# Performance work log

Hardware: AMD Instinct MI355X
Metric: run time of the kernel (lower is better)

The kernel has to match this reference:

```python
import jax, jax.numpy as jnp
import numpy as np

B, S, D, H, DH = 2, 2048, 1024, 16, 64
GLOBAL_RATIO = 0.1
LN_EPS = 1e-5


def setup_inputs() -> dict:
    key = jax.random.key(0)
    ks = jax.random.split(key, 8)
    w = lambda k, shape: jax.random.normal(k, shape, jnp.float32) * 0.02
    return {
        'x': jax.random.normal(ks[0], (B, S, D), jnp.float32),
        'Wq': w(ks[1], (D, H * DH)),
        'Wk': w(ks[2], (D, H * DH)),
        'Wv': w(ks[3], (D, H * DH)),
        'Wo': w(ks[4], (H * DH, D)),
        'bo': jnp.zeros((D,), jnp.float32),
        'ln_gamma': jnp.ones((DH,), jnp.float32),
        'ln_beta': jnp.zeros((DH,), jnp.float32),
        'Wg': w(ks[5], (2 * DH, DH)),
        'bg': jnp.zeros((DH,), jnp.float32),
    }


def _layernorm(x, gamma, beta):
    mu = jnp.mean(x, axis=-1, keepdims=True)
    var = jnp.mean(jnp.square(x - mu), axis=-1, keepdims=True)
    return (x - mu) * jax.lax.rsqrt(var + LN_EPS) * gamma + beta


def reference(x, Wq, Wk, Wv, Wo, bo, ln_gamma, ln_beta, Wg, bg):
    b, s, _ = x.shape
    # projections -> [b, h, n, d]
    split = lambda t: t.reshape(b, s, H, DH).transpose(0, 2, 1, 3)
    q = split(x @ Wq)
    k = split(x @ Wk)
    v = split(x @ Wv)
    scale = DH ** -0.5

    # local (full) attention: manual QK^T / softmax / AV
    scores = jnp.einsum('bhnd,bhmd->bhnm', q, k) * scale  # [b,h,s,s]
    attn = jax.nn.softmax(scores, axis=-1)
    local_out = jnp.einsum('bhnm,bhmd->bhnd', attn, v)

    # cross-segment fusion: top-k keys by norm per (b, h)
    num_global = max(1, int(s * GLOBAL_RATIO))
    key_norms = jnp.linalg.norm(k, axis=-1)  # [b,h,s]
    _, top_idx = jax.lax.top_k(key_norms, num_global)  # [b,h,g]
    idx = top_idx[..., None]  # [b,h,g,1]
    global_k = jnp.take_along_axis(k, idx, axis=2)  # [b,h,g,d]
    global_v = jnp.take_along_axis(v, idx, axis=2)
    g_scores = jnp.einsum('bhnd,bhgd->bhng', q, global_k) * scale
    g_attn = jax.nn.softmax(g_scores, axis=-1)
    global_out = jnp.einsum('bhng,bhgd->bhnd', g_attn, global_v)
    global_out = _layernorm(global_out, ln_gamma, ln_beta)

    # learned gate over [local, global]
    cat = jnp.concatenate([local_out, global_out], axis=-1)  # [b,h,s,2d]
    gate = jax.nn.sigmoid(cat @ Wg + bg)
    fused = gate * local_out + (1.0 - gate) * global_out

    out = fused.transpose(0, 2, 1, 3).reshape(b, s, H * DH)  # b h n d -> b n (h d)
    return out @ Wo + bo
```

## Files before the change

kernel.cpp:

```cpp
#include <hip/hip_runtime.h>


constexpr int SEQ    = 2048;
constexpr int DMODEL = 1024;
constexpr int NH     = 16;
constexpr int DHEAD  = 64;
constexpr int BHT    = 32;
constexpr int NG     = 204;
constexpr int NGPAD  = 256;
constexpr float LNEPS = 1e-5f;

typedef __attribute__((ext_vector_type(8))) short short8;
typedef __attribute__((ext_vector_type(4))) short short4v;
typedef __attribute__((ext_vector_type(4))) float f32x4;

__device__ __forceinline__ unsigned short f2bf(float f) {
    unsigned int u = __float_as_uint(f);
    u += 0x7FFFu + ((u >> 16) & 1u);
    return (unsigned short)(u >> 16);
}
__device__ __forceinline__ float bf2f(unsigned short b) {
    return __uint_as_float(((unsigned int)b) << 16);
}

__global__ __launch_bounds__(256)
void prep_k(const float* __restrict__ x,
            const float* __restrict__ Wq, const float* __restrict__ Wv,
            const float* __restrict__ Wo, const float* __restrict__ Wk,
            const float* __restrict__ Wg,
            unsigned short* __restrict__ xh, unsigned short* __restrict__ xl,
            unsigned short* __restrict__ Wqt, unsigned short* __restrict__ Wvt,
            unsigned short* __restrict__ Wot, unsigned short* __restrict__ Wkh,
            unsigned short* __restrict__ Wkl, unsigned short* __restrict__ Wgt)
{
    const int bid = blockIdx.x;
    const int tid = threadIdx.x;

    if (bid < 2048) {
        int i = (bid * 256 + tid) << 3;
        short8 h, l;
#pragma unroll
        for (int j = 0; j < 8; ++j) {
            float v = x[i + j];
            unsigned short hb = f2bf(v);
            h[j] = (short)hb;
            l[j] = (short)f2bf(v - bf2f(hb));
        }
        *(short8*)(xh + i) = h;
        *(short8*)(xl + i) = l;
        return;
    }
    if (bid == 3072) {
#pragma unroll
        for (int i = 0; i < 32; ++i) {
            int o = tid * 32 + i;
            int dg = o >> 7, jj = o & 127;
            Wgt[o] = f2bf(Wg[jj * 64 + dg]);
        }
        return;
    }

    __shared__ float tile[64][68];
    const int sub = bid - 2048;
    const int which = sub >> 8;
    const int b = sub & 255;
    const int n0 = (b & 15) * 64, k0 = (b >> 4) * 64;
    const float* W = (which == 0) ? Wq : (which == 1) ? Wv : (which == 2) ? Wo : Wk;
    const int Kd = DMODEL, Nd = DMODEL;

#pragma unroll
    for (int p = 0; p < 4; ++p) {
        int c = tid + (p << 8);
        int r = c >> 4, c4 = (c & 15) << 2;
        *(float4*)&tile[r][c4] = *(const float4*)(W + (size_t)(k0 + r) * Nd + n0 + c4);
    }
    __syncthreads();
#pragma unroll
    for (int p = 0; p < 4; ++p) {
        int c = tid + (p << 8);
        int n = c >> 4, k4 = (c & 15) << 2;
        if (which < 3) {
            unsigned short* Wt = (which == 0) ? Wqt : (which == 1) ? Wvt : Wot;
            short4v o;
#pragma unroll
            for (int j = 0; j < 4; ++j) o[j] = (short)f2bf(tile[k4 + j][n]);
            *(short4v*)(Wt + (size_t)(n0 + n) * Kd + k0 + k4) = o;
        } else {
            short4v oh, ol;
#pragma unroll
            for (int j = 0; j < 4; ++j) {
                float v = tile[k4 + j][n];
                unsigned short hb = f2bf(v);
                oh[j] = (short)hb;
                ol[j] = (short)f2bf(v - bf2f(hb));
            }
            *(short4v*)(Wkh + (size_t)(n0 + n) * Kd + k0 + k4) = oh;
            *(short4v*)(Wkl + (size_t)(n0 + n) * Kd + k0 + k4) = ol;
        }
    }
}

__global__ __launch_bounds__(512)
void gemm_bf16_k(const unsigned short* __restrict__ A,
                 const unsigned short* __restrict__ Bt,
                 const float* __restrict__ bias,
                 void* __restrict__ outv, void* __restrict__ outv2,
                 unsigned short* __restrict__ vtout,
                 int M, int N, int K, int mode)
{
    __shared__ __align__(16) unsigned short As[128][72];
    __shared__ __align__(16) unsigned short Bs[128][72];
    const int tid = threadIdx.x;
    const int lane = tid & 63, wave = tid >> 6;
    const int quad = lane >> 4, ln = lane & 15;
    const int mh = (wave >> 2) << 6;
    const int nh = (wave & 3) << 5;
    const int m0 = blockIdx.y * 128, n0 = blockIdx.x * 128;

    f32x4 acc[4][2];
#pragma unroll
    for (int i = 0; i < 4; ++i)
#pragma unroll
        for (int j = 0; j < 2; ++j) acc[i][j] = (f32x4){0.f, 0.f, 0.f, 0.f};

    short8 areg[2], breg[2];
#pragma unroll
    for (int p = 0; p < 2; ++p) {
        int c = tid + (p << 9);
        int row = c >> 3, col8 = (c & 7) << 3;
        areg[p] = *(const short8*)(A + (size_t)(m0 + row) * K + col8);
        breg[p] = *(const short8*)(Bt + (size_t)(n0 + row) * K + col8);
    }

    for (int k0 = 0; k0 < K; k0 += 64) {
        __syncthreads();
#pragma unroll
        for (int p = 0; p < 2; ++p) {
            int c = tid + (p << 9);
            int row = c >> 3, col8 = (c & 7) << 3;
            *(short8*)&As[row][col8] = areg[p];
            *(short8*)&Bs[row][col8] = breg[p];
        }
        __syncthreads();
        if (k0 + 64 < K) {
#pragma unroll
            for (int p = 0; p < 2; ++p) {
                int c = tid + (p << 9);
                int row = c >> 3, col8 = (c & 7) << 3;
                areg[p] = *(const short8*)(A + (size_t)(m0 + row) * K + k0 + 64 + col8);
                breg[p] = *(const short8*)(Bt + (size_t)(n0 + row) * K + k0 + 64 + col8);
            }
        }
#pragma unroll
        for (int ch = 0; ch < 2; ++ch) {
            short8 af[4], bf[2];
#pragma unroll
            for (int mt = 0; mt < 4; ++mt)
                af[mt] = *(const short8*)&As[mh + mt * 16 + ln][ch * 32 + quad * 8];
#pragma unroll
            for (int nt = 0; nt < 2; ++nt)
                bf[nt] = *(const short8*)&Bs[nh + nt * 16 + ln][ch * 32 + quad * 8];
#pragma unroll
            for (int mt = 0; mt < 4; ++mt)
#pragma unroll
                for (int nt = 0; nt < 2; ++nt)
                    acc[mt][nt] = __builtin_amdgcn_mfma_f32_16x16x32_bf16(
                        af[mt], bf[nt], acc[mt][nt], 0, 0, 0);
        }
    }

    if (mode == 0) {
        float* out = (float*)outv;
#pragma unroll
        for (int mt = 0; mt < 4; ++mt)
#pragma unroll
            for (int nt = 0; nt < 2; ++nt)
#pragma unroll
                for (int r = 0; r < 4; ++r) {
                    int m = m0 + mh + mt * 16 + quad * 4 + r;
                    int n = n0 + nh + nt * 16 + ln;
                    out[(size_t)m * N + n] = acc[mt][nt][r] + bias[n];
                }
    } else {
#pragma unroll
        for (int mt = 0; mt < 4; ++mt)
#pragma unroll
            for (int nt = 0; nt < 2; ++nt) {
                int n = n0 + nh + nt * 16 + ln;
                int mb = m0 + mh + mt * 16 + quad * 4;
                int b = mb >> 11, s0 = mb & (SEQ - 1);
                int d = n & 63;
                if (n < DMODEL) {
                    int h = n >> 6;
                    unsigned short* qp_ =
                        (unsigned short*)outv + ((size_t)(b * NH + h) * SEQ + s0) * DHEAD + d;
#pragma unroll
                    for (int r = 0; r < 4; ++r)
                        qp_[(size_t)r * DHEAD] = f2bf(acc[mt][nt][r] * 0.18033688f);
                } else {
                    int h = (n >> 6) - NH;
                    unsigned short* vp_ =
                        (unsigned short*)outv2 + ((size_t)(b * NH + h) * SEQ + s0) * DHEAD + d;
                    short4v tv;
#pragma unroll
                    for (int r = 0; r < 4; ++r) {
                        unsigned short bv = f2bf(acc[mt][nt][r]);
                        vp_[(size_t)r * DHEAD] = bv;
                        tv[r] = (short)bv;
                    }
                    *(short4v*)(vtout + ((size_t)(b * NH + h) * DHEAD + d) * SEQ + s0) = tv;
                }
            }
    }
}

__global__ __launch_bounds__(512)
void gemm_kproj_mfma(const unsigned short* __restrict__ xh,
                     const unsigned short* __restrict__ xl,
                     const unsigned short* __restrict__ Wh,
                     const unsigned short* __restrict__ Wl,
                     unsigned short* __restrict__ kout,
                     float* __restrict__ norms2)
{
    __shared__ __align__(16) unsigned short Ah[128][72];
    __shared__ __align__(16) unsigned short Al[128][72];
    __shared__ __align__(16) unsigned short Bh[128][72];
    __shared__ __align__(16) unsigned short Bl[128][72];
    const int K = DMODEL;
    const int tid = threadIdx.x;
    const int lane = tid & 63, wave = tid >> 6;
    const int quad = lane >> 4, ln = lane & 15;
    const int mh = (wave >> 1) << 5;
    const int nh = (wave & 1) << 6;
    const int m0 = blockIdx.y * 128, n0 = blockIdx.x * 128;

    f32x4 acc[2][4];
#pragma unroll
    for (int i = 0; i < 2; ++i)
#pragma unroll
        for (int j = 0; j < 4; ++j) acc[i][j] = (f32x4){0.f, 0.f, 0.f, 0.f};

    short8 ahreg[2], alreg[2], bhreg[2], blreg[2];
#pragma unroll
    for (int p = 0; p < 2; ++p) {
        int c = tid + (p << 9);
        int row = c >> 3, col8 = (c & 7) << 3;
        size_t ga = (size_t)(m0 + row) * K + col8;
        size_t gb = (size_t)(n0 + row) * K + col8;
        ahreg[p] = *(const short8*)(xh + ga);
        alreg[p] = *(const short8*)(xl + ga);
        bhreg[p] = *(const short8*)(Wh + gb);
        blreg[p] = *(const short8*)(Wl + gb);
    }

    for (int k0 = 0; k0 < K; k0 += 64) {
        __syncthreads();
#pragma unroll
        for (int p = 0; p < 2; ++p) {
            int c = tid + (p << 9);
            int row = c >> 3, col8 = (c & 7) << 3;
            *(short8*)&Ah[row][col8] = ahreg[p];
            *(short8*)&Al[row][col8] = alreg[p];
            *(short8*)&Bh[row][col8] = bhreg[p];
            *(short8*)&Bl[row][col8] = blreg[p];
        }
        __syncthreads();
        if (k0 + 64 < K) {
#pragma unroll
            for (int p = 0; p < 2; ++p) {
                int c = tid + (p << 9);
                int row = c >> 3, col8 = (c & 7) << 3;
                size_t ga = (size_t)(m0 + row) * K + k0 + 64 + col8;
                size_t gb = (size_t)(n0 + row) * K + k0 + 64 + col8;
                ahreg[p] = *(const short8*)(xh + ga);
                alreg[p] = *(const short8*)(xl + ga);
                bhreg[p] = *(const short8*)(Wh + gb);
                blreg[p] = *(const short8*)(Wl + gb);
            }
        }
#pragma unroll
        for (int ch = 0; ch < 2; ++ch) {
            short8 afh[2], afl[2];
#pragma unroll
            for (int mt = 0; mt < 2; ++mt) {
                afh[mt] = *(const short8*)&Ah[mh + mt * 16 + ln][ch * 32 + quad * 8];
                afl[mt] = *(const short8*)&Al[mh + mt * 16 + ln][ch * 32 + quad * 8];
            }
#pragma unroll
            for (int nt = 0; nt < 4; ++nt) {
                short8 bfh = *(const short8*)&Bh[nh + nt * 16 + ln][ch * 32 + quad * 8];
                short8 bfl = *(const short8*)&Bl[nh + nt * 16 + ln][ch * 32 + quad * 8];
#pragma unroll
                for (int mt = 0; mt < 2; ++mt) {
                    acc[mt][nt] = __builtin_amdgcn_mfma_f32_16x16x32_bf16(afh[mt], bfh, acc[mt][nt], 0, 0, 0);
                    acc[mt][nt] = __builtin_amdgcn_mfma_f32_16x16x32_bf16(afh[mt], bfl, acc[mt][nt], 0, 0, 0);
                    acc[mt][nt] = __builtin_amdgcn_mfma_f32_16x16x32_bf16(afl[mt], bfh, acc[mt][nt], 0, 0, 0);
                }
            }
        }
    }

    const int h = (n0 + nh) >> 6;
#pragma unroll
    for (int mt = 0; mt < 2; ++mt)
#pragma unroll
        for (int r = 0; r < 4; ++r) {
            int m = m0 + mh + mt * 16 + quad * 4 + r;
            int b = m >> 11, s = m & (SEQ - 1);
            size_t rowbase = ((size_t)(b * NH + h) * SEQ + s) * DHEAD;
#pragma unroll
            for (int nt = 0; nt < 4; ++nt)
                kout[rowbase + nt * 16 + ln] = f2bf(acc[mt][nt][r]);
            float s2 = acc[mt][0][r] * acc[mt][0][r] + acc[mt][1][r] * acc[mt][1][r] +
                       acc[mt][2][r] * acc[mt][2][r] + acc[mt][3][r] * acc[mt][3][r];
#pragma unroll
            for (int off = 1; off <= 8; off <<= 1)
                s2 += __shfl_xor(s2, off);
            if (ln == 0)
                norms2[(size_t)(b * NH + h) * SEQ + s] = s2;
        }
}

__global__ __launch_bounds__(512)
void topk_gather_k(const float* __restrict__ norms2,
                   const unsigned short* __restrict__ k,
                   const unsigned short* __restrict__ v,
                   unsigned short* __restrict__ gk,
                   unsigned short* __restrict__ gvt)
{
    __shared__ unsigned long long keys[SEQ];
    __shared__ int tix[NGPAD];
    __shared__ __align__(16) unsigned short T[64][72];
    const int bh = blockIdx.x;
    const int tid = threadIdx.x;
    const float* nb = norms2 + (size_t)bh * SEQ;
    const size_t base = (size_t)bh * SEQ * DHEAD;

    for (int i = tid; i < SEQ; i += 512) {
        float nrm = sqrtf(nb[i]);
        keys[i] = ((unsigned long long)__float_as_uint(nrm) << 32) |
                  (unsigned int)(0xFFFFFFFFu - (unsigned int)i);
    }
    __syncthreads();
    for (int kk = 2; kk <= SEQ; kk <<= 1) {
        for (int j = kk >> 1; j > 0; j >>= 1) {
            for (int i = tid; i < SEQ; i += 512) {
                int ixj = i ^ j;
                if (ixj > i) {
                    unsigned long long a = keys[i], b = keys[ixj];
                    bool up = ((i & kk) == 0);
                    if ((a > b) == up) { keys[i] = b; keys[ixj] = a; }
                }
            }
            __syncthreads();
        }
    }
    if (tid < NGPAD) {
        tix[tid] = (tid < NG)
            ? (int)(0xFFFFFFFFu - (unsigned int)(keys[SEQ - 1 - tid] & 0xFFFFFFFFu))
            : 0;
    }
    __syncthreads();

    for (int t = 0; t < NGPAD / 64; ++t) {
        {
            int idx = tid;
            int row = idx >> 3, col8 = (idx & 7) << 3;
            int g = t * 64 + row;
            short8 kv = (short8)0, vv = (short8)0;
            if (g < NG) {
                int sidx = tix[g];
                kv = *(const short8*)(k + base + (size_t)sidx * DHEAD + col8);
                vv = *(const short8*)(v + base + (size_t)sidx * DHEAD + col8);
            }
            *(short8*)(gk + ((size_t)bh * NGPAD + g) * DHEAD + col8) = kv;
            *(short8*)&T[row][col8] = vv;
        }
        __syncthreads();
        {
            int idx = tid;
            int d = idx >> 3, k8 = (idx & 7) << 3;
            short8 o;
#pragma unroll
            for (int i = 0; i < 8; ++i) o[i] = (short)T[k8 + i][d];
            *(short8*)(gvt + ((size_t)bh * DHEAD + d) * NGPAD + t * 64 + k8) = o;
        }
        __syncthreads();
    }
}

__global__ __launch_bounds__(256, 2)
void attn_fused_k(const unsigned short* __restrict__ qb,
                  const unsigned short* __restrict__ kb,
                  const unsigned short* __restrict__ vt,
                  const unsigned short* __restrict__ gk,
                  const unsigned short* __restrict__ gvt,
                  const unsigned short* __restrict__ Wgt,
                  const float* __restrict__ gamma,
                  const float* __restrict__ beta,
                  const float* __restrict__ bg,
                  unsigned short* __restrict__ fused)
{
    __shared__ __align__(16) unsigned short smem[27136];
    unsigned short* const KsB = smem;
    unsigned short* const VtB = smem + 9216;
    unsigned short (*Ps)[72]  = (unsigned short (*)[72])smem;
    unsigned short (*Wgs)[136] = (unsigned short (*)[136])(smem + 18432);

    const int flat = blockIdx.x;
    const int bh = ((flat >> 7) << 3) | (flat & 7);
    const int q0 = ((flat >> 3) & 15) * 128;
    const int tid = threadIdx.x;
    const int lane = tid & 63, wave = tid >> 6;
    const int quad = lane >> 4, ln = lane & 15;
    const size_t base = (size_t)bh * SEQ * DHEAD;
    const unsigned short* gkb = gk + (size_t)bh * NGPAD * DHEAD;
    const unsigned short* gvb = gvt + (size_t)bh * DHEAD * NGPAD;

#pragma unroll
    for (int p = 0; p < 4; ++p) {
        int idx = tid + (p << 8);
        *(short8*)&Wgs[idx >> 4][(idx & 15) << 3] = *(const short8*)(Wgt + idx * 8);
    }

    short8 qf[2][2];
#pragma unroll
    for (int mt = 0; mt < 2; ++mt) {
        const unsigned short* qp = qb + base + (size_t)(q0 + wave * 32 + mt * 16 + ln) * DHEAD;
        qf[mt][0] = *(const short8*)(qp + quad * 8);
        qf[mt][1] = *(const short8*)(qp + 32 + quad * 8);
    }

    f32x4 O[2][4], Og[2][4];
#pragma unroll
    for (int mt = 0; mt < 2; ++mt)
#pragma unroll
        for (int nt = 0; nt < 4; ++nt) {
            O[mt][nt] = (f32x4){0.f, 0.f, 0.f, 0.f};
            Og[mt][nt] = (f32x4){0.f, 0.f, 0.f, 0.f};
        }
    float ls[2] = {0.f, 0.f}, lg[2] = {0.f, 0.f};

    short8 kreg[2], vreg[2];
    int srow[2], scol8[2], psrow[2];
#pragma unroll
    for (int p = 0; p < 2; ++p) {
        int idx = tid + (p << 8);
        srow[p] = idx >> 3;
        scol8[p] = (idx & 7) << 3;
        psrow[p] = (srow[p] & 0x20) | ((srow[p] & 0x0C) << 1) |
                   ((srow[p] & 0x10) >> 2) | (srow[p] & 3);
    }

    auto loadT = [&](int i) {
#pragma unroll
        for (int p = 0; p < 2; ++p) {
            if (i < 32) {
                kreg[p] = *(const short8*)(kb + base + (size_t)(i * 64 + psrow[p]) * DHEAD + scol8[p]);
                vreg[p] = *(const short8*)(vt + base + (size_t)srow[p] * SEQ + i * 64 + scol8[p]);
            } else {
                int g = i - 32;
                kreg[p] = *(const short8*)(gkb + (size_t)(g * 64 + psrow[p]) * DHEAD + scol8[p]);
                vreg[p] = *(const short8*)(gvb + (size_t)srow[p] * NGPAD + g * 64 + scol8[p]);
            }
        }
    };
    auto storeT = [&](int buf) {
        unsigned short* kd = KsB + buf * 4608;
        unsigned short* vd = VtB + buf * 4608;
#pragma unroll
        for (int p = 0; p < 2; ++p) {
            *(short8*)&kd[srow[p] * 72 + scol8[p]] = kreg[p];
            *(short8*)&vd[srow[p] * 72 + scol8[p]] = vreg[p];
        }
    };

    loadT(0);
    storeT(0);
    loadT(1);
    __syncthreads();

    for (int t = 0; t < 32; ++t) {
        const int cur = t & 1;
        const unsigned short* Kc = KsB + cur * 4608;
        const unsigned short* Vc = VtB + cur * 4608;

        f32x4 s[2][4];
#pragma unroll
        for (int mt = 0; mt < 2; ++mt)
#pragma unroll
            for (int nt = 0; nt < 4; ++nt) s[mt][nt] = (f32x4){0.f, 0.f, 0.f, 0.f};
        __builtin_amdgcn_s_setprio(1);
#pragma unroll
        for (int nt = 0; nt < 4; ++nt) {
            short8 kf0 = *(const short8*)&Kc[(nt * 16 + ln) * 72 + quad * 8];
            short8 kf1 = *(const short8*)&Kc[(nt * 16 + ln) * 72 + 32 + quad * 8];
#pragma unroll
            for (int mt = 0; mt < 2; ++mt) {
                s[mt][nt] = __builtin_amdgcn_mfma_f32_16x16x32_bf16(kf0, qf[mt][0], s[mt][nt], 0, 0, 0);
                s[mt][nt] = __builtin_amdgcn_mfma_f32_16x16x32_bf16(kf1, qf[mt][1], s[mt][nt], 0, 0, 0);
            }
        }
        __builtin_amdgcn_s_setprio(0);

        short8 pf8[2][2];
#pragma unroll
        for (int mt = 0; mt < 2; ++mt)
#pragma unroll
            for (int nt = 0; nt < 4; ++nt)
#pragma unroll
                for (int r = 0; r < 4; ++r) {
                    unsigned int u = __float_as_uint(__builtin_amdgcn_exp2f(s[mt][nt][r]));
                    ls[mt] += __uint_as_float(u & 0xFFFF0000u);
                    pf8[mt][nt >> 1][((nt & 1) << 2) | r] = (short)(u >> 16);
                }

        __builtin_amdgcn_s_setprio(1);
#pragma unroll
        for (int dt = 0; dt < 4; ++dt)
#pragma unroll
            for (int c = 0; c < 2; ++c) {
                short8 vf = *(const short8*)&Vc[(dt * 16 + ln) * 72 + c * 32 + quad * 8];
#pragma unroll
                for (int mt = 0; mt < 2; ++mt)
                    O[mt][dt] = __builtin_amdgcn_mfma_f32_16x16x32_bf16(
                        pf8[mt][c], vf, O[mt][dt], 0, 0, 0);
            }
        __builtin_amdgcn_s_setprio(0);

        storeT(cur ^ 1);
        if (t + 2 <= 35) loadT(t + 2);
        __syncthreads();
    }

    for (int tg = 0; tg < 4; ++tg) {
        const int t = 32 + tg;
        const int cur = t & 1;
        const unsigned short* Kc = KsB + cur * 4608;
        const unsigned short* Vc = VtB + cur * 4608;

        f32x4 s[2][4];
#pragma unroll
        for (int mt = 0; mt < 2; ++mt)
#pragma unroll
            for (int nt = 0; nt < 4; ++nt) s[mt][nt] = (f32x4){0.f, 0.f, 0.f, 0.f};
        __builtin_amdgcn_s_setprio(1);
#pragma unroll
        for (int nt = 0; nt < 4; ++nt) {
            short8 kf0 = *(const short8*)&Kc[(nt * 16 + ln) * 72 + quad * 8];
            short8 kf1 = *(const short8*)&Kc[(nt * 16 + ln) * 72 + 32 + quad * 8];
#pragma unroll
            for (int mt = 0; mt < 2; ++mt) {
                s[mt][nt] = __builtin_amdgcn_mfma_f32_16x16x32_bf16(kf0, qf[mt][0], s[mt][nt], 0, 0, 0);
                s[mt][nt] = __builtin_amdgcn_mfma_f32_16x16x32_bf16(kf1, qf[mt][1], s[mt][nt], 0, 0, 0);
            }
        }
        __builtin_amdgcn_s_setprio(0);

        short8 pf8[2][2];
#pragma unroll
        for (int nt = 0; nt < 4; ++nt)
#pragma unroll
            for (int r = 0; r < 4; ++r) {
                int phi = ((nt >> 1) << 5) | (quad << 3) | ((nt & 1) << 2) | r;
                bool valid = (tg * 64 + phi) < NG;
#pragma unroll
                for (int mt = 0; mt < 2; ++mt) {
                    float p = valid ? __builtin_amdgcn_exp2f(s[mt][nt][r]) : 0.f;
                    unsigned int u = __float_as_uint(p);
                    lg[mt] += __uint_as_float(u & 0xFFFF0000u);
                    pf8[mt][nt >> 1][((nt & 1) << 2) | r] = (short)(u >> 16);
                }
            }

        __builtin_amdgcn_s_setprio(1);
#pragma unroll
        for (int dt = 0; dt < 4; ++dt)
#pragma unroll
            for (int c = 0; c < 2; ++c) {
                short8 vf = *(const short8*)&Vc[(dt * 16 + ln) * 72 + c * 32 + quad * 8];
#pragma unroll
                for (int mt = 0; mt < 2; ++mt)
                    Og[mt][dt] = __builtin_amdgcn_mfma_f32_16x16x32_bf16(
                        pf8[mt][c], vf, Og[mt][dt], 0, 0, 0);
            }
        __builtin_amdgcn_s_setprio(0);

        if (t < 35) storeT(cur ^ 1);
        if (t + 2 <= 35) loadT(t + 2);
        __syncthreads();
    }

#pragma unroll
    for (int mt = 0; mt < 2; ++mt) {
        ls[mt] += __shfl_xor(ls[mt], 16);
        ls[mt] += __shfl_xor(ls[mt], 32);
        lg[mt] += __shfl_xor(lg[mt], 16);
        lg[mt] += __shfl_xor(lg[mt], 32);
    }
    float invl[2][4], invg[2][4];
#pragma unroll
    for (int mt = 0; mt < 2; ++mt)
#pragma unroll
        for (int r = 0; r < 4; ++r) {
            invl[mt][r] = 1.f / __shfl(ls[mt], quad * 4 + r);
            invg[mt][r] = 1.f / __shfl(lg[mt], quad * 4 + r);
        }

    float xs[2][4][4];
#pragma unroll
    for (int mt = 0; mt < 2; ++mt)
#pragma unroll
        for (int r = 0; r < 4; ++r) {
            float inv = invg[mt][r];
#pragma unroll
            for (int nt = 0; nt < 4; ++nt) xs[mt][nt][r] = Og[mt][nt][r] * inv;
        }
    float mu[2][4], rsd[2][4];
#pragma unroll
    for (int mt = 0; mt < 2; ++mt)
#pragma unroll
        for (int r = 0; r < 4; ++r) {
            float sm = xs[mt][0][r] + xs[mt][1][r] + xs[mt][2][r] + xs[mt][3][r];
#pragma unroll
            for (int off = 1; off <= 8; off <<= 1) sm += __shfl_xor(sm, off);
            mu[mt][r] = sm * (1.f / 64.f);
        }
#pragma unroll
    for (int mt = 0; mt < 2; ++mt)
#pragma unroll
        for (int r = 0; r < 4; ++r) {
            float sv = 0.f;
#pragma unroll
            for (int nt = 0; nt < 4; ++nt) {
                float d = xs[mt][nt][r] - mu[mt][r];
                sv += d * d;
            }
#pragma unroll
            for (int off = 1; off <= 8; off <<= 1) sv += __shfl_xor(sv, off);
            rsd[mt][r] = rsqrtf(sv * (1.f / 64.f) + LNEPS);
        }
#pragma unroll
    for (int nt = 0; nt < 4; ++nt) {
        float g = gamma[nt * 16 + ln], bb = beta[nt * 16 + ln];
#pragma unroll
        for (int mt = 0; mt < 2; ++mt)
#pragma unroll
            for (int r = 0; r < 4; ++r)
                xs[mt][nt][r] = (xs[mt][nt][r] - mu[mt][r]) * rsd[mt][r] * g + bb;
    }

    float lf[2][4][4];
#pragma unroll
    for (int mt = 0; mt < 2; ++mt)
#pragma unroll
        for (int nt = 0; nt < 4; ++nt)
#pragma unroll
            for (int r = 0; r < 4; ++r) {
                lf[mt][nt][r] = O[mt][nt][r] * invl[mt][r];
                Ps[wave * 32 + mt * 16 + quad * 4 + r][nt * 16 + ln] = f2bf(lf[mt][nt][r]);
            }
    f32x4 gacc[2][4];
#pragma unroll
    for (int ng = 0; ng < 4; ++ng) {
        float bgv = bg[ng * 16 + ln];
#pragma unroll
        for (int mt = 0; mt < 2; ++mt)
            gacc[mt][ng] = (f32x4){bgv, bgv, bgv, bgv};
    }
#pragma unroll
    for (int ch = 0; ch < 2; ++ch) {
        short8 af[2];
#pragma unroll
        for (int mt = 0; mt < 2; ++mt)
            af[mt] = *(const short8*)&Ps[wave * 32 + mt * 16 + ln][ch * 32 + quad * 8];
#pragma unroll
        for (int ng = 0; ng < 4; ++ng) {
            short8 bf = *(const short8*)&Wgs[ng * 16 + ln][ch * 32 + quad * 8];
#pragma unroll
            for (int mt = 0; mt < 2; ++mt)
                gacc[mt][ng] = __builtin_amdgcn_mfma_f32_16x16x32_bf16(af[mt], bf, gacc[mt][ng], 0, 0, 0);
        }
    }
#pragma unroll
    for (int mt = 0; mt < 2; ++mt)
#pragma unroll
        for (int nt = 0; nt < 4; ++nt)
#pragma unroll
            for (int r = 0; r < 4; ++r)
                Ps[wave * 32 + mt * 16 + quad * 4 + r][nt * 16 + ln] = f2bf(xs[mt][nt][r]);
#pragma unroll
    for (int ch = 0; ch < 2; ++ch) {
        short8 af[2];
#pragma unroll
        for (int mt = 0; mt < 2; ++mt)
            af[mt] = *(const short8*)&Ps[wave * 32 + mt * 16 + ln][ch * 32 + quad * 8];
#pragma unroll
        for (int ng = 0; ng < 4; ++ng) {
            short8 bf = *(const short8*)&Wgs[ng * 16 + ln][64 + ch * 32 + quad * 8];
#pragma unroll
            for (int mt = 0; mt < 2; ++mt)
                gacc[mt][ng] = __builtin_amdgcn_mfma_f32_16x16x32_bf16(af[mt], bf, gacc[mt][ng], 0, 0, 0);
        }
    }

    const int b = bh >> 4, h = bh & 15;
#pragma unroll
    for (int mt = 0; mt < 2; ++mt)
#pragma unroll
        for (int ng = 0; ng < 4; ++ng)
#pragma unroll
            for (int r = 0; r < 4; ++r) {
                float gt = 1.f / (1.f + __expf(-gacc[mt][ng][r]));
                float f = gt * lf[mt][ng][r] + (1.f - gt) * xs[mt][ng][r];
                int s = q0 + wave * 32 + mt * 16 + quad * 4 + r;
                fused[((size_t)(b * SEQ + s)) * DMODEL + h * DHEAD + ng * 16 + ln] = f2bf(f);
            }
}

extern "C" void kernel_launch(void* const* d_in, const int* in_sizes, int n_in,
                              void* d_out, int out_size, void* d_ws, size_t ws_size,
                              hipStream_t stream)
{
    (void)in_sizes; (void)n_in; (void)out_size; (void)ws_size;
    const float* x    = (const float*)d_in[0];
    const float* Wq   = (const float*)d_in[1];
    const float* Wk   = (const float*)d_in[2];
    const float* Wv   = (const float*)d_in[3];
    const float* Wo   = (const float*)d_in[4];
    const float* bo   = (const float*)d_in[5];
    const float* ln_g = (const float*)d_in[6];
    const float* ln_b = (const float*)d_in[7];
    const float* Wg   = (const float*)d_in[8];
    const float* bg   = (const float*)d_in[9];

    char* w = (char*)d_ws;
    const size_t MB = 1024ull * 1024ull;
    unsigned short* kb16  = (unsigned short*)(w);
    unsigned short* qb16  = (unsigned short*)(w + 8 * MB);
    unsigned short* vb16  = (unsigned short*)(w + 16 * MB);
    unsigned short* vt16  = (unsigned short*)(w + 24 * MB);
    unsigned short* xh    = (unsigned short*)(w + 32 * MB);
    unsigned short* xl    = (unsigned short*)(w + 40 * MB);
    unsigned short* Wqt   = (unsigned short*)(w + 48 * MB);
    unsigned short* Wvt   = (unsigned short*)(w + 50 * MB);
    unsigned short* Wot   = (unsigned short*)(w + 52 * MB);
    unsigned short* Wkh   = (unsigned short*)(w + 54 * MB);
    unsigned short* Wkl   = (unsigned short*)(w + 56 * MB);
    unsigned short* Wgt   = (unsigned short*)(w + 58 * MB);
    float*          norms2= (float*)(w + 59 * MB);
    unsigned short* gk16  = (unsigned short*)(w + 60 * MB);
    unsigned short* gvt16 = (unsigned short*)(w + 61 * MB);
    unsigned short* fusedb = xh;

    const int M = 4096, N = 1024, K = 1024;

    prep_k<<<3073, 256, 0, stream>>>(x, Wq, Wv, Wo, Wk, Wg,
                                     xh, xl, Wqt, Wvt, Wot, Wkh, Wkl, Wgt);

    dim3 gqv(2048 / 128, M / 128);
    gemm_bf16_k<<<gqv, 512, 0, stream>>>(xh, Wqt, nullptr, qb16, vb16, vt16,
                                         M, 2048, K, 3);

    dim3 gkp(N / 128, M / 128);
    gemm_kproj_mfma<<<gkp, 512, 0, stream>>>(xh, xl, Wkh, Wkl, kb16, norms2);

    topk_gather_k<<<BHT, 512, 0, stream>>>(norms2, kb16, vb16, gk16, gvt16);

    attn_fused_k<<<512, 256, 0, stream>>>(qb16, kb16, vt16, gk16, gvt16, Wgt,
                                          ln_g, ln_b, bg, fusedb);

    dim3 go_(N / 128, M / 128);
    gemm_bf16_k<<<go_, 512, 0, stream>>>(fusedb, Wot, bo, (float*)d_out, nullptr,
                                         nullptr, M, N, K, 0);
}
```

Before: 265.2 us.

## Merge Q/V and K projection GEMMs into one launch; compute softmax sums via MFMA

```diff
diff --git a/kernel.cpp b/kernel.cpp
--- a/kernel.cpp
+++ b/kernel.cpp
@@ -104,9 +104,8 @@
 void gemm_bf16_k(const unsigned short* __restrict__ A,
                  const unsigned short* __restrict__ Bt,
                  const float* __restrict__ bias,
-                 void* __restrict__ outv, void* __restrict__ outv2,
-                 unsigned short* __restrict__ vtout,
-                 int M, int N, int K, int mode)
+                 float* __restrict__ out,
+                 int M, int N, int K)
 {
     __shared__ __align__(16) unsigned short As[128][72];
     __shared__ __align__(16) unsigned short Bs[128][72];
@@ -169,19 +168,96 @@
         }
     }
 
-    if (mode == 0) {
-        float* out = (float*)outv;
-#pragma unroll
-        for (int mt = 0; mt < 4; ++mt)
-#pragma unroll
-            for (int nt = 0; nt < 2; ++nt)
-#pragma unroll
-                for (int r = 0; r < 4; ++r) {
-                    int m = m0 + mh + mt * 16 + quad * 4 + r;
-                    int n = n0 + nh + nt * 16 + ln;
-                    out[(size_t)m * N + n] = acc[mt][nt][r] + bias[n];
+#pragma unroll
+    for (int mt = 0; mt < 4; ++mt)
+#pragma unroll
+        for (int nt = 0; nt < 2; ++nt)
+#pragma unroll
+            for (int r = 0; r < 4; ++r) {
+                int m = m0 + mh + mt * 16 + quad * 4 + r;
+                int n = n0 + nh + nt * 16 + ln;
+                out[(size_t)m * N + n] = acc[mt][nt][r] + bias[n];
+            }
+}
+
+__global__ __launch_bounds__(512)
+void proj_qvk_k(const unsigned short* __restrict__ xh,
+                const unsigned short* __restrict__ xl,
+                const unsigned short* __restrict__ Wqt,
+                const unsigned short* __restrict__ Wkh,
+                const unsigned short* __restrict__ Wkl,
+                unsigned short* __restrict__ qb,
+                unsigned short* __restrict__ vb,
+                unsigned short* __restrict__ vtout,
+                unsigned short* __restrict__ kout,
+                float* __restrict__ norms2)
+{
+    __shared__ __align__(16) unsigned short smem[36864];
+    const int blk = blockIdx.x;
+    const int tid = threadIdx.x;
+    const int lane = tid & 63, wave = tid >> 6;
+    const int quad = lane >> 4, ln = lane & 15;
+    const int K = DMODEL;
+
+    if (blk < 512) {
+        unsigned short* As = smem;
+        unsigned short* Bs = smem + 9216;
+        const int m0 = (blk >> 4) * 128, n0 = (blk & 15) * 128;
+        const int mh = (wave >> 2) << 6;
+        const int nh = (wave & 3) << 5;
+
+        f32x4 acc[4][2];
+#pragma unroll
+        for (int i = 0; i < 4; ++i)
+#pragma unroll
+            for (int j = 0; j < 2; ++j) acc[i][j] = (f32x4){0.f, 0.f, 0.f, 0.f};
+
+        short8 areg[2], breg[2];
+#pragma unroll
+        for (int p = 0; p < 2; ++p) {
+            int c = tid + (p << 9);
+            int row = c >> 3, col8 = (c & 7) << 3;
+            areg[p] = *(const short8*)(xh + (size_t)(m0 + row) * K + col8);
+            breg[p] = *(const short8*)(Wqt + (size_t)(n0 + row) * K + col8);
+        }
+
+        for (int k0 = 0; k0 < K; k0 += 64) {
+            __syncthreads();
+#pragma unroll
+            for (int p = 0; p < 2; ++p) {
+                int c = tid + (p << 9);
+                int row = c >> 3, col8 = (c & 7) << 3;
+                *(short8*)&As[row * 72 + col8] = areg[p];
+                *(short8*)&Bs[row * 72 + col8] = breg[p];
+            }
+            __syncthreads();
+            if (k0 + 64 < K) {
+#pragma unroll
+                for (int p = 0; p < 2; ++p) {
+                    int c = tid + (p << 9);
+                    int row = c >> 3, col8 = (c & 7) << 3;
+                    areg[p] = *(const short8*)(xh + (size_t)(m0 + row) * K + k0 + 64 + col8);
+                    breg[p] = *(const short8*)(Wqt + (size_t)(n0 + row) * K + k0 + 64 + col8);
                 }
-    } else {
+            }
+#pragma unroll
+            for (int ch = 0; ch < 2; ++ch) {
+                short8 af[4], bf[2];
+#pragma unroll
+                for (int mt = 0; mt < 4; ++mt)
+                    af[mt] = *(const short8*)&As[(mh + mt * 16 + ln) * 72 + ch * 32 + quad * 8];
+#pragma unroll
+                for (int nt = 0; nt < 2; ++nt)
+                    bf[nt] = *(const short8*)&Bs[(nh + nt * 16 + ln) * 72 + ch * 32 + quad * 8];
+#pragma unroll
+                for (int mt = 0; mt < 4; ++mt)
+#pragma unroll
+                    for (int nt = 0; nt < 2; ++nt)
+                        acc[mt][nt] = __builtin_amdgcn_mfma_f32_16x16x32_bf16(
+                            af[mt], bf[nt], acc[mt][nt], 0, 0, 0);
+            }
+        }
+
 #pragma unroll
         for (int mt = 0; mt < 4; ++mt)
 #pragma unroll
@@ -193,14 +269,14 @@
                 if (n < DMODEL) {
                     int h = n >> 6;
                     unsigned short* qp_ =
-                        (unsigned short*)outv + ((size_t)(b * NH + h) * SEQ + s0) * DHEAD + d;
+                        qb + ((size_t)(b * NH + h) * SEQ + s0) * DHEAD + d;
 #pragma unroll
                     for (int r = 0; r < 4; ++r)
                         qp_[(size_t)r * DHEAD] = f2bf(acc[mt][nt][r] * 0.18033688f);
                 } else {
                     int h = (n >> 6) - NH;
                     unsigned short* vp_ =
-                        (unsigned short*)outv2 + ((size_t)(b * NH + h) * SEQ + s0) * DHEAD + d;
+                        vb + ((size_t)(b * NH + h) * SEQ + s0) * DHEAD + d;
                     short4v tv;
 #pragma unroll
                     for (int r = 0; r < 4; ++r) {
@@ -211,114 +287,102 @@
                     *(short4v*)(vtout + ((size_t)(b * NH + h) * DHEAD + d) * SEQ + s0) = tv;
                 }
             }
-    }
-}
-
-__global__ __launch_bounds__(512)
-void gemm_kproj_mfma(const unsigned short* __restrict__ xh,
-                     const unsigned short* __restrict__ xl,
-                     const unsigned short* __restrict__ Wh,
-                     const unsigned short* __restrict__ Wl,
-                     unsigned short* __restrict__ kout,
-                     float* __restrict__ norms2)
-{
-    __shared__ __align__(16) unsigned short Ah[128][72];
-    __shared__ __align__(16) unsigned short Al[128][72];
-    __shared__ __align__(16) unsigned short Bh[128][72];
-    __shared__ __align__(16) unsigned short Bl[128][72];
-    const int K = DMODEL;
-    const int tid = threadIdx.x;
-    const int lane = tid & 63, wave = tid >> 6;
-    const int quad = lane >> 4, ln = lane & 15;
-    const int mh = (wave >> 1) << 5;
-    const int nh = (wave & 1) << 6;
-    const int m0 = blockIdx.y * 128, n0 = blockIdx.x * 128;
-
-    f32x4 acc[2][4];
-#pragma unroll
-    for (int i = 0; i < 2; ++i)
-#pragma unroll
-        for (int j = 0; j < 4; ++j) acc[i][j] = (f32x4){0.f, 0.f, 0.f, 0.f};
-
-    short8 ahreg[2], alreg[2], bhreg[2], blreg[2];
-#pragma unroll
-    for (int p = 0; p < 2; ++p) {
-        int c = tid + (p << 9);
-        int row = c >> 3, col8 = (c & 7) << 3;
-        size_t ga = (size_t)(m0 + row) * K + col8;
-        size_t gb = (size_t)(n0 + row) * K + col8;
-        ahreg[p] = *(const short8*)(xh + ga);
-        alreg[p] = *(const short8*)(xl + ga);
-        bhreg[p] = *(const short8*)(Wh + gb);
-        blreg[p] = *(const short8*)(Wl + gb);
-    }
-
-    for (int k0 = 0; k0 < K; k0 += 64) {
-        __syncthreads();
+    } else {
+        unsigned short* Ah = smem;
+        unsigned short* Al = smem + 9216;
+        unsigned short* Bh = smem + 18432;
+        unsigned short* Bl = smem + 27648;
+        const int sb = blk - 512;
+        const int m0 = (sb >> 3) * 128, n0 = (sb & 7) * 128;
+        const int mh = (wave >> 1) << 5;
+        const int nh = (wave & 1) << 6;
+
+        f32x4 acc[2][4];
+#pragma unroll
+        for (int i = 0; i < 2; ++i)
+#pragma unroll
+            for (int j = 0; j < 4; ++j) acc[i][j] = (f32x4){0.f, 0.f, 0.f, 0.f};
+
+        short8 ahreg[2], alreg[2], bhreg[2], blreg[2];
 #pragma unroll
         for (int p = 0; p < 2; ++p) {
             int c = tid + (p << 9);
             int row = c >> 3, col8 = (c & 7) << 3;
-            *(short8*)&Ah[row][col8] = ahreg[p];
-            *(short8*)&Al[row][col8] = alreg[p];
-            *(short8*)&Bh[row][col8] = bhreg[p];
-            *(short8*)&Bl[row][col8] = blreg[p];
-        }
-        __syncthreads();
-        if (k0 + 64 < K) {
+            size_t ga = (size_t)(m0 + row) * K + col8;
+            size_t gb = (size_t)(n0 + row) * K + col8;
+            ahreg[p] = *(const short8*)(xh + ga);
+            alreg[p] = *(const short8*)(xl + ga);
+            bhreg[p] = *(const short8*)(Wkh + gb);
+            blreg[p] = *(const short8*)(Wkl + gb);
+        }
+
+        for (int k0 = 0; k0 < K; k0 += 64) {
+            __syncthreads();
 #pragma unroll
             for (int p = 0; p < 2; ++p) {
                 int c = tid + (p << 9);
                 int row = c >> 3, col8 = (c & 7) << 3;
-                size_t ga = (size_t)(m0 + row) * K + k0 + 64 + col8;
-                size_t gb = (size_t)(n0 + row) * K + k0 + 64 + col8;
-                ahreg[p] = *(const short8*)(xh + ga);
-                alreg[p] = *(const short8*)(xl + ga);
-                bhreg[p] = *(const short8*)(Wh + gb);
-                blreg[p] = *(const short8*)(Wl + gb);
-            }
-        }
-#pragma unroll
-        for (int ch = 0; ch < 2; ++ch) {
-            short8 afh[2], afl[2];
-#pragma unroll
-            for (int mt = 0; mt < 2; ++mt) {
-                afh[mt] = *(const short8*)&Ah[mh + mt * 16 + ln][ch * 32 + quad * 8];
-                afl[mt] = *(const short8*)&Al[mh + mt * 16 + ln][ch * 32 + quad * 8];
-            }
-#pragma unroll
-            for (int nt = 0; nt < 4; ++nt) {
-                short8 bfh = *(const short8*)&Bh[nh + nt * 16 + ln][ch * 32 + quad * 8];
-                short8 bfl = *(const short8*)&Bl[nh + nt * 16 + ln][ch * 32 + quad * 8];
+                *(short8*)&Ah[row * 72 + col8] = ahreg[p];
+                *(short8*)&Al[row * 72 + col8] = alreg[p];
+                *(short8*)&Bh[row * 72 + col8] = bhreg[p];
+                *(short8*)&Bl[row * 72 + col8] = blreg[p];
+            }
+            __syncthreads();
+            if (k0 + 64 < K) {
+#pragma unroll
+                for (int p = 0; p < 2; ++p) {
+                    int c = tid + (p << 9);
+                    int row = c >> 3, col8 = (c & 7) << 3;
+                    size_t ga = (size_t)(m0 + row) * K + k0 + 64 + col8;
+                    size_t gb = (size_t)(n0 + row) * K + k0 + 64 + col8;
+                    ahreg[p] = *(const short8*)(xh + ga);
+                    alreg[p] = *(const short8*)(xl + ga);
+                    bhreg[p] = *(const short8*)(Wkh + gb);
+                    blreg[p] = *(const short8*)(Wkl + gb);
+                }
+            }
+#pragma unroll
+            for (int ch = 0; ch < 2; ++ch) {
+                short8 afh[2], afl[2];
 #pragma unroll
                 for (int mt = 0; mt < 2; ++mt) {
-                    acc[mt][nt] = __builtin_amdgcn_mfma_f32_16x16x32_bf16(afh[mt], bfh, acc[mt][nt], 0, 0, 0);
-                    acc[mt][nt] = __builtin_amdgcn_mfma_f32_16x16x32_bf16(afh[mt], bfl, acc[mt][nt], 0, 0, 0);
-                    acc[mt][nt] = __builtin_amdgcn_mfma_f32_16x16x32_bf16(afl[mt], bfh, acc[mt][nt], 0, 0, 0);
+                    afh[mt] = *(const short8*)&Ah[(mh + mt * 16 + ln) * 72 + ch * 32 + quad * 8];
+                    afl[mt] = *(const short8*)&Al[(mh + mt * 16 + ln) * 72 + ch * 32 + quad * 8];
                 }
-            }
-        }
-    }
-
-    const int h = (n0 + nh) >> 6;
-#pragma unroll
-    for (int mt = 0; mt < 2; ++mt)
-#pragma unroll
-        for (int r = 0; r < 4; ++r) {
-            int m = m0 + mh + mt * 16 + quad * 4 + r;
-            int b = m >> 11, s = m & (SEQ - 1);
-            size_t rowbase = ((size_t)(b * NH + h) * SEQ + s) * DHEAD;
-#pragma unroll
-            for (int nt = 0; nt < 4; ++nt)
-                kout[rowbase + nt * 16 + ln] = f2bf(acc[mt][nt][r]);
-            float s2 = acc[mt][0][r] * acc[mt][0][r] + acc[mt][1][r] * acc[mt][1][r] +
-                       acc[mt][2][r] * acc[mt][2][r] + acc[mt][3][r] * acc[mt][3][r];
-#pragma unroll
-            for (int off = 1; off <= 8; off <<= 1)
-                s2 += __shfl_xor(s2, off);
-            if (ln == 0)
-                norms2[(size_t)(b * NH + h) * SEQ + s] = s2;
-        }
+#pragma unroll
+                for (int nt = 0; nt < 4; ++nt) {
+                    short8 bfh = *(const short8*)&Bh[(nh + nt * 16 + ln) * 72 + ch * 32 + quad * 8];
+                    short8 bfl = *(const short8*)&Bl[(nh + nt * 16 + ln) * 72 + ch * 32 + quad * 8];
+#pragma unroll
+                    for (int mt = 0; mt < 2; ++mt) {
+                        acc[mt][nt] = __builtin_amdgcn_mfma_f32_16x16x32_bf16(afh[mt], bfh, acc[mt][nt], 0, 0, 0);
+                        acc[mt][nt] = __builtin_amdgcn_mfma_f32_16x16x32_bf16(afh[mt], bfl, acc[mt][nt], 0, 0, 0);
+                        acc[mt][nt] = __builtin_amdgcn_mfma_f32_16x16x32_bf16(afl[mt], bfh, acc[mt][nt], 0, 0, 0);
+                    }
+                }
+            }
+        }
+
+        const int h = (n0 + nh) >> 6;
+#pragma unroll
+        for (int mt = 0; mt < 2; ++mt)
+#pragma unroll
+            for (int r = 0; r < 4; ++r) {
+                int m = m0 + mh + mt * 16 + quad * 4 + r;
+                int b = m >> 11, s = m & (SEQ - 1);
+                size_t rowbase = ((size_t)(b * NH + h) * SEQ + s) * DHEAD;
+#pragma unroll
+                for (int nt = 0; nt < 4; ++nt)
+                    kout[rowbase + nt * 16 + ln] = f2bf(acc[mt][nt][r]);
+                float s2 = acc[mt][0][r] * acc[mt][0][r] + acc[mt][1][r] * acc[mt][1][r] +
+                           acc[mt][2][r] * acc[mt][2][r] + acc[mt][3][r] * acc[mt][3][r];
+#pragma unroll
+                for (int off = 1; off <= 8; off <<= 1)
+                    s2 += __shfl_xor(s2, off);
+                if (ln == 0)
+                    norms2[(size_t)(b * NH + h) * SEQ + s] = s2;
+            }
+    }
 }
 
 __global__ __launch_bounds__(512)
@@ -431,15 +495,24 @@
         qf[mt][1] = *(const short8*)(qp + 32 + quad * 8);
     }
 
-    f32x4 O[2][4], Og[2][4];
-#pragma unroll
-    for (int mt = 0; mt < 2; ++mt)
+    short8 onesv, maskv;
+#pragma unroll
+    for (int j = 0; j < 8; ++j) {
+        onesv[j] = (short)0x3F80;
+        maskv[j] = (short)((quad * 8 + j) < 12 ? 0x3F80 : 0);
+    }
+
+    f32x4 O[2][4], Og[2][4], lsacc[2], lgacc[2];
+#pragma unroll
+    for (int mt = 0; mt < 2; ++mt) {
 #pragma unroll
         for (int nt = 0; nt < 4; ++nt) {
             O[mt][nt] = (f32x4){0.f, 0.f, 0.f, 0.f};
             Og[mt][nt] = (f32x4){0.f, 0.f, 0.f, 0.f};
         }
-    float ls[2] = {0.f, 0.f}, lg[2] = {0.f, 0.f};
+        lsacc[mt] = (f32x4){0.f, 0.f, 0.f, 0.f};
+        lgacc[mt] = (f32x4){0.f, 0.f, 0.f, 0.f};
+    }
 
     short8 kreg[2], vreg[2];
     int srow[2], scol8[2], psrow[2];
@@ -511,7 +584,6 @@
 #pragma unroll
                 for (int r = 0; r < 4; ++r) {
                     unsigned int u = __float_as_uint(__builtin_amdgcn_exp2f(s[mt][nt][r]));
-                    ls[mt] += __uint_as_float(u & 0xFFFF0000u);
                     pf8[mt][nt >> 1][((nt & 1) << 2) | r] = (short)(u >> 16);
                 }
 
@@ -526,6 +598,12 @@
                     O[mt][dt] = __builtin_amdgcn_mfma_f32_16x16x32_bf16(
                         pf8[mt][c], vf, O[mt][dt], 0, 0, 0);
             }
+#pragma unroll
+        for (int c = 0; c < 2; ++c)
+#pragma unroll
+            for (int mt = 0; mt < 2; ++mt)
+                lsacc[mt] = __builtin_amdgcn_mfma_f32_16x16x32_bf16(
+                    pf8[mt][c], onesv, lsacc[mt], 0, 0, 0);
         __builtin_amdgcn_s_setprio(0);
 
         storeT(cur ^ 1);
@@ -559,19 +637,14 @@
 
         short8 pf8[2][2];
 #pragma unroll
-        for (int nt = 0; nt < 4; ++nt)
-#pragma unroll
-            for (int r = 0; r < 4; ++r) {
-                int phi = ((nt >> 1) << 5) | (quad << 3) | ((nt & 1) << 2) | r;
-                bool valid = (tg * 64 + phi) < NG;
-#pragma unroll
-                for (int mt = 0; mt < 2; ++mt) {
-                    float p = valid ? __builtin_amdgcn_exp2f(s[mt][nt][r]) : 0.f;
-                    unsigned int u = __float_as_uint(p);
-                    lg[mt] += __uint_as_float(u & 0xFFFF0000u);
+        for (int mt = 0; mt < 2; ++mt)
+#pragma unroll
+            for (int nt = 0; nt < 4; ++nt)
+#pragma unroll
+                for (int r = 0; r < 4; ++r) {
+                    unsigned int u = __float_as_uint(__builtin_amdgcn_exp2f(s[mt][nt][r]));
                     pf8[mt][nt >> 1][((nt & 1) << 2) | r] = (short)(u >> 16);
                 }
-            }
 
         __builtin_amdgcn_s_setprio(1);
 #pragma unroll
@@ -584,6 +657,19 @@
                     Og[mt][dt] = __builtin_amdgcn_mfma_f32_16x16x32_bf16(
                         pf8[mt][c], vf, Og[mt][dt], 0, 0, 0);
             }
+        if (tg < 3) {
+#pragma unroll
+            for (int c = 0; c < 2; ++c)
+#pragma unroll
+                for (int mt = 0; mt < 2; ++mt)
+                    lgacc[mt] = __builtin_amdgcn_mfma_f32_16x16x32_bf16(
+                        pf8[mt][c], onesv, lgacc[mt], 0, 0, 0);
+        } else {
+#pragma unroll
+            for (int mt = 0; mt < 2; ++mt)
+                lgacc[mt] = __builtin_amdgcn_mfma_f32_16x16x32_bf16(
+                    pf8[mt][0], maskv, lgacc[mt], 0, 0, 0);
+        }
         __builtin_amdgcn_s_setprio(0);
 
         if (t < 35) storeT(cur ^ 1);
@@ -591,20 +677,13 @@
         __syncthreads();
     }
 
-#pragma unroll
-    for (int mt = 0; mt < 2; ++mt) {
-        ls[mt] += __shfl_xor(ls[mt], 16);
-        ls[mt] += __shfl_xor(ls[mt], 32);
-        lg[mt] += __shfl_xor(lg[mt], 16);
-        lg[mt] += __shfl_xor(lg[mt], 32);
-    }
     float invl[2][4], invg[2][4];
 #pragma unroll
     for (int mt = 0; mt < 2; ++mt)
 #pragma unroll
         for (int r = 0; r < 4; ++r) {
-            invl[mt][r] = 1.f / __shfl(ls[mt], quad * 4 + r);
-            invg[mt][r] = 1.f / __shfl(lg[mt], quad * 4 + r);
+            invl[mt][r] = 1.f / lsacc[mt][r];
+            invg[mt][r] = 1.f / lgacc[mt][r];
         }
 
     float xs[2][4][4];
@@ -752,18 +831,15 @@
     unsigned short* gk16  = (unsigned short*)(w + 60 * MB);
     unsigned short* gvt16 = (unsigned short*)(w + 61 * MB);
     unsigned short* fusedb = xh;
+    (void)Wvt;
 
     const int M = 4096, N = 1024, K = 1024;
 
     prep_k<<<3073, 256, 0, stream>>>(x, Wq, Wv, Wo, Wk, Wg,
                                      xh, xl, Wqt, Wvt, Wot, Wkh, Wkl, Wgt);
 
-    dim3 gqv(2048 / 128, M / 128);
-    gemm_bf16_k<<<gqv, 512, 0, stream>>>(xh, Wqt, nullptr, qb16, vb16, vt16,
-                                         M, 2048, K, 3);
-
-    dim3 gkp(N / 128, M / 128);
-    gemm_kproj_mfma<<<gkp, 512, 0, stream>>>(xh, xl, Wkh, Wkl, kb16, norms2);
+    proj_qvk_k<<<768, 512, 0, stream>>>(xh, xl, Wqt, Wkh, Wkl,
+                                        qb16, vb16, vt16, kb16, norms2);
 
     topk_gather_k<<<BHT, 512, 0, stream>>>(norms2, kb16, vb16, gk16, gvt16);
 
@@ -771,6 +847,6 @@
                                           ln_g, ln_b, bg, fusedb);
 
     dim3 go_(N / 128, M / 128);
-    gemm_bf16_k<<<go_, 512, 0, stream>>>(fusedb, Wot, bo, (float*)d_out, nullptr,
-                                         nullptr, M, N, K, 0);
+    gemm_bf16_k<<<go_, 512, 0, stream>>>(fusedb, Wot, bo, (float*)d_out,
+                                         M, N, K);
 }
```

New measurement: 257.2 us. 3.0% less time.
